# Kernel optimization log

Measured on AMD Instinct MI355X. Metric: run time of the kernel, lower is better.

Reference implementation:

```python
import jax, jax.numpy as jnp
from jax import lax
import numpy as np

C = 64          # in_channel
CL = 32         # latent channels = in_channel // latent_dim
IC = 32         # inter_channel
GH, GW = 8, 8   # grid


def conv1x1(x, W, b):
    # x: [N,C,H,W], W: [O,C], b: [O]
    return jnp.einsum('nchw,oc->nohw', x, W) + b[None, :, None, None]


def maxpool2(x):
    return lax.reduce_window(x, -jnp.inf, lax.max, (1, 1, 2, 2), (1, 1, 2, 2), 'VALID')


def conv3x3(x, W, b):
    y = lax.conv_general_dilated(x, W, (1, 1), ((1, 1), (1, 1)),
                                 dimension_numbers=('NCHW', 'OIHW', 'NCHW'))
    return y + b[None, :, None, None]


def setup_inputs() -> dict:
    key = jax.random.key(0)
    ks = jax.random.split(key, 20)
    s = 0.05
    inp = {
        'x': jax.random.normal(ks[0], (4, C, 256, 256), jnp.float32),
        # Self_Attn_FM params (1x1 convs stored as matrices)
        'Wq': jax.random.normal(ks[1], (CL, C), jnp.float32) * s,
        'bq': jnp.zeros((CL,), jnp.float32),
        'Wk': jax.random.normal(ks[2], (CL, C), jnp.float32) * s,
        'bk': jnp.zeros((CL,), jnp.float32),
        'Wv': jax.random.normal(ks[3], (CL, C), jnp.float32) * s,
        'bv': jnp.zeros((CL,), jnp.float32),
        'Wo': jax.random.normal(ks[4], (C, CL), jnp.float32) * s,
        'bo': jnp.zeros((C,), jnp.float32),
        'gamma': jax.random.normal(ks[5], ()) * 0.5,
        # dense conv blocks: dims 64 -> 96 -> 128, each -> 32
        'W1': jax.random.normal(ks[6], (IC, C, 3, 3), jnp.float32) * s,
        'b1': jnp.zeros((IC,), jnp.float32),
        'W2': jax.random.normal(ks[7], (IC, C + IC, 3, 3), jnp.float32) * s,
        'b2': jnp.zeros((IC,), jnp.float32),
        'W3': jax.random.normal(ks[8], (IC, C + 2 * IC, 3, 3), jnp.float32) * s,
        'b3': jnp.zeros((IC,), jnp.float32),
        # fusion 1x1: (C + 3*IC) -> C
        'Wf': jax.random.normal(ks[9], (C, C + 3 * IC), jnp.float32) * s,
        'bf': jnp.zeros((C,), jnp.float32),
    }
    return inp


def region_non_local(x, Wq, bq, Wk, bk, Wv, bv, Wo, bo, gamma):
    B, Cc, H, W = x.shape
    h, w = H // GH, W // GW
    # split into grid cells, batched: [B*GH*GW, C, h, w]
    cells = x.reshape(B, Cc, GH, h, GW, w).transpose(0, 2, 4, 1, 3, 5)
    cells = cells.reshape(B * GH * GW, Cc, h, w)
    N, L = cells.shape[0], h * w
    q = conv1x1(cells, Wq, bq).reshape(N, CL, L)                 # [N,c,L]
    k = maxpool2(conv1x1(cells, Wk, bk)).reshape(N, CL, L // 4)  # [N,c,L/4]
    v = maxpool2(conv1x1(cells, Wv, bv)).reshape(N, CL, L // 4)
    attn = jax.nn.softmax(jnp.einsum('ncq,nck->nqk', q, k), axis=-1)
    out = jnp.einsum('nck,nqk->ncq', v, attn).reshape(N, CL, h, w)
    out = gamma * conv1x1(out, Wo, bo) + cells
    # regroup cells back to [B,C,H,W]
    out = out.reshape(B, GH, GW, Cc, h, w).transpose(0, 3, 1, 4, 2, 5)
    return out.reshape(B, Cc, H, W)


def reference(x, Wq, bq, Wk, bk, Wv, bv, Wo, bo, gamma,
              W1, b1, W2, b2, W3, b3, Wf, bf):
    f0 = region_non_local(x, Wq, bq, Wk, bk, Wv, bv, Wo, bo, gamma)
    f1 = jax.nn.relu(conv3x3(f0, W1, b1))
    f2 = jax.nn.relu(conv3x3(jnp.concatenate([f0, f1], axis=1), W2, b2))
    f3 = jax.nn.relu(conv3x3(jnp.concatenate([f0, f1, f2], axis=1), W3, b3))
    cat = jnp.concatenate([f0, f1, f2, f3], axis=1)
    out = conv1x1(cat, Wf, bf) + x
    return out
```

## Files before the change

kernel.cpp:

```cpp
#include <hip/hip_runtime.h>


typedef short s16x8 __attribute__((ext_vector_type(8)));
typedef float f32x4 __attribute__((ext_vector_type(4)));
typedef unsigned short ushort_t;

__device__ __forceinline__ unsigned short f2bf(float f) {
  union { float f; unsigned int u; } v; v.f = f;
  unsigned int r = v.u + 0x7fffu + ((v.u >> 16) & 1u);
  return (unsigned short)(r >> 16);
}
__device__ __forceinline__ float bf2f(unsigned short h) {
  union { unsigned int u; float f; } v; v.u = ((unsigned int)h) << 16;
  return v.f;
}

__global__ void repack_kernel(const float* __restrict__ W1, const float* __restrict__ W2,
                              const float* __restrict__ W3, const float* __restrict__ Wf,
                              ushort_t* __restrict__ wc1, ushort_t* __restrict__ wc2,
                              ushort_t* __restrict__ wc3, ushort_t* __restrict__ wff)
{
  const int i = blockIdx.x * 256 + threadIdx.x;
  if (i < 18432) {
    int j = i & 7, o = (i >> 3) & 31, r = i >> 8, tap = r >> 3, kg = r & 7;
    wc1[i] = f2bf(W1[o * 576 + (kg * 8 + j) * 9 + tap]);
  }
  if (i < 27648) {
    int j = i & 7, o = (i >> 3) & 31, r = i >> 8, tap = r / 12, kg = r % 12;
    wc2[i] = f2bf(W2[o * 864 + (kg * 8 + j) * 9 + tap]);
  }
  if (i < 36864) {
    int j = i & 7, o = (i >> 3) & 31, r = i >> 8, tap = r >> 4, kg = r & 15;
    wc3[i] = f2bf(W3[o * 1152 + (kg * 8 + j) * 9 + tap]);
  }
  if (i < 10240) {
    int j = i & 7, o = (i >> 3) & 63, kg = i >> 9;
    wff[i] = f2bf(Wf[o * 160 + kg * 8 + j]);
  }
}

__global__ __launch_bounds__(256, 4) void kvx_kernel(
    const float* __restrict__ x,
    const float* __restrict__ Wk, const float* __restrict__ bk,
    const float* __restrict__ Wv, const float* __restrict__ bv,
    ushort_t* __restrict__ xt, ushort_t* __restrict__ kg, ushort_t* __restrict__ vt)
{
  __shared__ __attribute__((aligned(16))) ushort_t lds[64 * 258];
  __shared__ ushort_t kvs[4][8][64];

  const int bid = blockIdx.x;
  const int n   = bid >> 8;
  const int rem = bid & 255;
  const int pr  = rem >> 1;
  const int xh  = rem & 1;
  const int tid = threadIdx.x, lane = tid & 63, wv = tid >> 6;
  const int quad = lane >> 4, l15 = lane & 15;

  const int y0 = pr * 2;
  const int x0 = xh * 128;
  const int gh = pr >> 4, pyc = pr & 15;

  const float* xblk = x + (size_t)n * (64 * 65536) + (size_t)(y0 * 256 + x0);
  ushort_t*    xtn  = xt + (size_t)n * (65536 * 64);

#pragma unroll 4
  for (int i = 0; i < 16; ++i) {
    const int idx = (i << 8) + tid;
    const int c  = idx >> 6;
    const int r  = (idx >> 5) & 1;
    const int sg = idx & 31;
    const f32x4 v = *(const f32x4*)(xblk + (size_t)c * 65536 + r * 256 + sg * 4);
    const unsigned int lo = (unsigned int)f2bf(v[0]) | ((unsigned int)f2bf(v[1]) << 16);
    const unsigned int hi = (unsigned int)f2bf(v[2]) | ((unsigned int)f2bf(v[3]) << 16);
    const int base = c * 258 + (r << 7) + (sg << 2);
    *(unsigned int*)&lds[base]     = lo;
    *(unsigned int*)&lds[base + 2] = hi;
  }

  s16x8 wkf[2][2], wvf[2][2];
#pragma unroll
  for (int ks = 0; ks < 2; ++ks)
#pragma unroll
    for (int nt = 0; nt < 2; ++nt) {
      const int off = (nt * 16 + l15) * 64 + ks * 32 + quad * 8;
      s16x8 tk, tv;
#pragma unroll
      for (int j = 0; j < 8; ++j) {
        tk[j] = (short)f2bf(Wk[off + j]);
        tv[j] = (short)f2bf(Wv[off + j]);
      }
      wkf[ks][nt] = tk; wvf[ks][nt] = tv;
    }
  float bkv[2], bvv[2];
#pragma unroll
  for (int nt = 0; nt < 2; ++nt) {
    bkv[nt] = bk[nt * 16 + l15];
    bvv[nt] = bv[nt * 16 + l15];
  }

  __syncthreads();

  {
    const int g  = lane & 7;
    const int pa = lane >> 3;
#pragma unroll
    for (int s = 0; s < 8; ++s) {
      const int p = (wv << 6) + (s << 3) + pa;
      s16x8 v;
#pragma unroll
      for (int j = 0; j < 8; ++j) v[j] = (short)lds[(g * 8 + j) * 258 + p];
      const int P = (y0 + (p >> 7)) * 256 + x0 + (p & 127);
      *(s16x8*)(xtn + (size_t)P * 64 + g * 8) = v;
    }
  }

  const f32x4 zf = {0.f, 0.f, 0.f, 0.f};
#pragma unroll
  for (int tt = 0; tt < 2; ++tt) {
    const int t   = wv * 2 + tt;
    const int px0 = t * 16 + l15;

    s16x8 a[2][2];
#pragma unroll
    for (int r = 0; r < 2; ++r)
#pragma unroll
      for (int ks = 0; ks < 2; ++ks) {
        s16x8 v;
#pragma unroll
        for (int j = 0; j < 8; ++j)
          v[j] = (short)lds[(ks * 32 + quad * 8 + j) * 258 + (r << 7) + px0];
        a[r][ks] = v;
      }

    f32x4 kd[2][2], vd[2][2];
#pragma unroll
    for (int r = 0; r < 2; ++r)
#pragma unroll
      for (int nt = 0; nt < 2; ++nt) {
        f32x4 k0 = __builtin_amdgcn_mfma_f32_16x16x32_bf16(a[r][0], wkf[0][nt], zf, 0, 0, 0);
        kd[r][nt] = __builtin_amdgcn_mfma_f32_16x16x32_bf16(a[r][1], wkf[1][nt], k0, 0, 0, 0);
        f32x4 v0 = __builtin_amdgcn_mfma_f32_16x16x32_bf16(a[r][0], wvf[0][nt], zf, 0, 0, 0);
        vd[r][nt] = __builtin_amdgcn_mfma_f32_16x16x32_bf16(a[r][1], wvf[1][nt], v0, 0, 0, 0);
      }

#pragma unroll
    for (int nt = 0; nt < 2; ++nt)
#pragma unroll
      for (int rr = 0; rr < 2; ++rr) {
        const float kp = fmaxf(fmaxf(kd[0][nt][2 * rr], kd[0][nt][2 * rr + 1]),
                               fmaxf(kd[1][nt][2 * rr], kd[1][nt][2 * rr + 1])) + bkv[nt];
        const float vp = fmaxf(fmaxf(vd[0][nt][2 * rr], vd[0][nt][2 * rr + 1]),
                               fmaxf(vd[1][nt][2 * rr], vd[1][nt][2 * rr + 1])) + bvv[nt];
        kvs[wv][quad * 2 + rr][nt * 16 + l15]      = f2bf(kp);
        kvs[wv][quad * 2 + rr][32 + nt * 16 + l15] = f2bf(vp);
      }

    const int gw    = xh * 4 + (t >> 1);
    const int cell  = (n << 6) + (gh << 3) + gw;
    const int kposb = pyc * 16 + (t & 1) * 8;
    if (lane < 32) {
      const s16x8 vv = *(const s16x8*)&kvs[wv][lane >> 2][(lane & 3) * 8];
      *(s16x8*)(kg + ((size_t)(cell << 8) + kposb + (lane >> 2)) * 32 + (lane & 3) * 8) = vv;
    } else {
      const int ch = lane - 32;
      s16x8 vv;
#pragma unroll
      for (int r = 0; r < 8; ++r) vv[r] = (short)kvs[wv][r][32 + ch];
      *(s16x8*)(vt + (size_t)(cell << 13) + ch * 256 + kposb) = vv;
    }
  }
}

__global__ __launch_bounds__(256, 3) void attn_kernel(
    const ushort_t* __restrict__ xt, const ushort_t* __restrict__ kg,
    const ushort_t* __restrict__ vt,
    const float* __restrict__ Wq, const float* __restrict__ bq,
    const float* __restrict__ Wo, const float* __restrict__ bo,
    const float* __restrict__ gamma_p, ushort_t* __restrict__ f0)
{
  __shared__ __attribute__((aligned(16))) ushort_t kl[256 * 36];
  __shared__ __attribute__((aligned(16))) ushort_t vl[32 * 260];
  __shared__ __attribute__((aligned(16))) ushort_t un[4][2176];

  const int bid = blockIdx.x;
  const int cell = bid >> 2;
  const int part = bid & 3;
  const int tid = threadIdx.x, lane = tid & 63, wv = tid >> 6;
  const int quad = lane >> 4, l15 = lane & 15;

  const int n  = cell >> 6;
  const int gh = (cell >> 3) & 7;
  const int gw = cell & 7;
  const int y0 = gh * 32, xc0 = gw * 32;

  const ushort_t* xtn = xt + (size_t)n * (65536 * 64);
  ushort_t*       f0n = f0 + (size_t)n * (65536 * 64);
  const ushort_t* kc  = kg + (size_t)(cell << 8) * 32;
  const ushort_t* vc  = vt + (size_t)(cell << 13);

  for (int idx = tid; idx < 1024; idx += 256) {
    const int kpos = idx >> 2, cg = idx & 3;
    *(s16x8*)&kl[kpos * 36 + cg * 8] = *(const s16x8*)(kc + kpos * 32 + cg * 8);
  }
  for (int idx = tid; idx < 1024; idx += 256) {
    const int ch = idx >> 5, seg = idx & 31;
    *(s16x8*)&vl[ch * 260 + seg * 8] = *(const s16x8*)(vc + ch * 256 + seg * 8);
  }

  const float gamma = gamma_p[0];

  s16x8 wqf[2][2];
#pragma unroll
  for (int ks = 0; ks < 2; ++ks)
#pragma unroll
    for (int nt = 0; nt < 2; ++nt) {
      const float* p = Wq + (nt * 16 + l15) * 64 + ks * 32 + quad * 8;
      s16x8 t;
#pragma unroll
      for (int j = 0; j < 8; ++j) t[j] = (short)f2bf(p[j]);
      wqf[ks][nt] = t;
    }
  s16x8 wof[4];
#pragma unroll
  for (int nt = 0; nt < 4; ++nt) {
    const float* p = Wo + (nt * 16 + l15) * 32 + quad * 8;
    s16x8 t;
#pragma unroll
    for (int j = 0; j < 8; ++j) t[j] = (short)f2bf(p[j]);
    wof[nt] = t;
  }
  float bqv[2]; bqv[0] = bq[l15]; bqv[1] = bq[16 + l15];
  float bov[4];
#pragma unroll
  for (int nt = 0; nt < 4; ++nt) bov[nt] = bo[nt * 16 + l15];

  __syncthreads();

  ushort_t* uw = un[wv];
  const f32x4 zf = {0.f, 0.f, 0.f, 0.f};

#pragma unroll 1
  for (int it = 0; it < 4; ++it) {
    const int mt = part * 16 + wv * 4 + it;
    const int pbase = mt * 16;

    const int p = pbase + l15;
    const int yy = p >> 5, xx = p & 31;
    const size_t pixg = (size_t)((y0 + yy) * 256 + xc0 + xx);

    const s16x8 a0 = *(const s16x8*)(xtn + pixg * 64 + quad * 8);
    const s16x8 a1 = *(const s16x8*)(xtn + pixg * 64 + 32 + quad * 8);
    f32x4 qd0 = zf, qd1 = zf;
    qd0 = __builtin_amdgcn_mfma_f32_16x16x32_bf16(a0, wqf[0][0], qd0, 0, 0, 0);
    qd0 = __builtin_amdgcn_mfma_f32_16x16x32_bf16(a1, wqf[1][0], qd0, 0, 0, 0);
    qd1 = __builtin_amdgcn_mfma_f32_16x16x32_bf16(a0, wqf[0][1], qd1, 0, 0, 0);
    qd1 = __builtin_amdgcn_mfma_f32_16x16x32_bf16(a1, wqf[1][1], qd1, 0, 0, 0);
#pragma unroll
    for (int i = 0; i < 4; ++i) {
      uw[(quad * 4 + i) * 40 + l15]      = f2bf(qd0[i] + bqv[0]);
      uw[(quad * 4 + i) * 40 + 16 + l15] = f2bf(qd1[i] + bqv[1]);
    }
    const s16x8 qa = *(const s16x8*)&uw[l15 * 40 + quad * 8];

    f32x4 S[16];
#pragma unroll
    for (int nt = 0; nt < 16; ++nt) {
      const s16x8 kb = *(const s16x8*)&kl[(nt * 16 + l15) * 36 + quad * 8];
      S[nt] = __builtin_amdgcn_mfma_f32_16x16x32_bf16(qa, kb, zf, 0, 0, 0);
    }

    float rl[4];
#pragma unroll
    for (int i = 0; i < 4; ++i) {
      float m = S[0][i];
#pragma unroll
      for (int nt = 1; nt < 16; ++nt) m = fmaxf(m, S[nt][i]);
#pragma unroll
      for (int d2 = 1; d2 < 16; d2 <<= 1) m = fmaxf(m, __shfl_xor(m, d2, 64));
      float s = 0.f;
#pragma unroll
      for (int nt = 0; nt < 16; ++nt) {
        float e = __expf(S[nt][i] - m);
        S[nt][i] = e;
        s += e;
      }
#pragma unroll
      for (int d2 = 1; d2 < 16; d2 <<= 1) s += __shfl_xor(s, d2, 64);
      rl[i] = s;
    }

    f32x4 O0 = zf, O1 = zf;
#pragma unroll
    for (int hh = 0; hh < 2; ++hh) {
#pragma unroll
      for (int t = 0; t < 8; ++t)
#pragma unroll
        for (int i = 0; i < 4; ++i)
          uw[(quad * 4 + i) * 136 + t * 16 + l15] = f2bf(S[hh * 8 + t][i]);
#pragma unroll
      for (int kk = 0; kk < 4; ++kk) {
        const s16x8 pa = *(const s16x8*)&uw[l15 * 136 + kk * 32 + quad * 8];
        const int kb0 = hh * 128 + kk * 32 + quad * 8;
        const s16x8 vb0 = *(const s16x8*)&vl[l15 * 260 + kb0];
        const s16x8 vb1 = *(const s16x8*)&vl[(16 + l15) * 260 + kb0];
        O0 = __builtin_amdgcn_mfma_f32_16x16x32_bf16(pa, vb0, O0, 0, 0, 0);
        O1 = __builtin_amdgcn_mfma_f32_16x16x32_bf16(pa, vb1, O1, 0, 0, 0);
      }
    }

#pragma unroll
    for (int i = 0; i < 4; ++i) {
      const float inv = 1.0f / rl[i];
      uw[(quad * 4 + i) * 40 + l15]      = f2bf(O0[i] * inv);
      uw[(quad * 4 + i) * 40 + 16 + l15] = f2bf(O1[i] * inv);
    }
    const s16x8 oa = *(const s16x8*)&uw[l15 * 40 + quad * 8];
#pragma unroll
    for (int nt = 0; nt < 4; ++nt) {
      f32x4 D = __builtin_amdgcn_mfma_f32_16x16x32_bf16(oa, wof[nt], zf, 0, 0, 0);
#pragma unroll
      for (int i = 0; i < 4; ++i)
        uw[(quad * 4 + i) * 72 + nt * 16 + l15] = f2bf(gamma * (D[i] + bov[nt]));
    }

    {
      const s16x8 fv0 = *(const s16x8*)&uw[l15 * 72 + quad * 16];
      const s16x8 fv1 = *(const s16x8*)&uw[l15 * 72 + quad * 16 + 8];
      const s16x8 xv0 = *(const s16x8*)(xtn + pixg * 64 + quad * 16);
      const s16x8 xv1 = *(const s16x8*)(xtn + pixg * 64 + quad * 16 + 8);
      s16x8 r0, r1;
#pragma unroll
      for (int j = 0; j < 8; ++j) {
        r0[j] = (short)f2bf(bf2f((unsigned short)fv0[j]) + bf2f((unsigned short)xv0[j]));
        r1[j] = (short)f2bf(bf2f((unsigned short)fv1[j]) + bf2f((unsigned short)xv1[j]));
      }
      *(s16x8*)(f0n + pixg * 64 + quad * 16)     = r0;
      *(s16x8*)(f0n + pixg * 64 + quad * 16 + 8) = r1;
    }
  }
}

template <int NCHUNK>
__global__ __launch_bounds__(256) void conv3_kernel(
    const ushort_t* __restrict__ s0, const ushort_t* __restrict__ s1,
    const ushort_t* __restrict__ s2, const ushort_t* __restrict__ wc,
    const float* __restrict__ bias, ushort_t* __restrict__ outp)
{
  __shared__ __attribute__((aligned(16))) ushort_t tile[612 * 40];

  const int bid = blockIdx.x;
  const int n = bid >> 7;
  const int t = bid & 127;
  const int ty0 = (t >> 3) * 16;
  const int tx0 = (t & 7) * 32;
  const int tid = threadIdx.x, lane = tid & 63, wv = tid >> 6;
  const int quad = lane >> 4, l15 = lane & 15;
  constexpr int Kg = NCHUNK * 4;

  const f32x4 zf = {0.f, 0.f, 0.f, 0.f};
  f32x4 acc[4][2][2];
#pragma unroll
  for (int r = 0; r < 4; ++r)
#pragma unroll
    for (int h = 0; h < 2; ++h) { acc[r][h][0] = zf; acc[r][h][1] = zf; }

  for (int ch = 0; ch < NCHUNK; ++ch) {
    const ushort_t* src; int cstr, cbase;
    if (ch < 2)       { src = s0 + (size_t)n * (65536 * 64); cstr = 64; cbase = ch * 32; }
    else if (ch == 2) { src = s1 + (size_t)n * (65536 * 32); cstr = 32; cbase = 0; }
    else              { src = s2 + (size_t)n * (65536 * 32); cstr = 32; cbase = 0; }

    __syncthreads();
    for (int u = tid; u < 2448; u += 256) {
      const int pix = u >> 2, cg = u & 3;
      const int lr = pix / 34, lc = pix - lr * 34;
      const int gy = ty0 - 1 + lr, gx = tx0 - 1 + lc;
      s16x8 v = {0, 0, 0, 0, 0, 0, 0, 0};
      if ((unsigned)gy < 256u && (unsigned)gx < 256u)
        v = *(const s16x8*)(src + (size_t)(gy * 256 + gx) * cstr + cbase + cg * 8);
      *(s16x8*)&tile[pix * 40 + cg * 8] = v;
    }
    __syncthreads();

#pragma unroll
    for (int tap = 0; tap < 9; ++tap) {
      const int ky = tap / 3, kx = tap - ky * 3;
      const ushort_t* wb = wc + ((size_t)(tap * Kg + ch * 4 + quad) * 32 + l15) * 8;
      const s16x8 b0 = *(const s16x8*)wb;
      const s16x8 b1 = *(const s16x8*)(wb + 128);
#pragma unroll
      for (int r = 0; r < 4; ++r) {
        const int lr = 4 * wv + r + ky;
#pragma unroll
        for (int h = 0; h < 2; ++h) {
          const int lc = h * 16 + l15 + kx;
          const s16x8 a = *(const s16x8*)&tile[(lr * 34 + lc) * 40 + quad * 8];
          acc[r][h][0] = __builtin_amdgcn_mfma_f32_16x16x32_bf16(a, b0, acc[r][h][0], 0, 0, 0);
          acc[r][h][1] = __builtin_amdgcn_mfma_f32_16x16x32_bf16(a, b1, acc[r][h][1], 0, 0, 0);
        }
      }
    }
  }

  const float bv0 = bias[l15], bv1 = bias[16 + l15];
  ushort_t* on = outp + (size_t)n * (65536 * 32);
#pragma unroll
  for (int r = 0; r < 4; ++r) {
    const int gy = ty0 + 4 * wv + r;
#pragma unroll
    for (int h = 0; h < 2; ++h) {
#pragma unroll
      for (int i = 0; i < 4; ++i) {
        const int gx = tx0 + h * 16 + quad * 4 + i;
        ushort_t* op = on + (size_t)(gy * 256 + gx) * 32;
        op[l15]      = f2bf(fmaxf(acc[r][h][0][i] + bv0, 0.f));
        op[16 + l15] = f2bf(fmaxf(acc[r][h][1][i] + bv1, 0.f));
      }
    }
  }
}

__global__ __launch_bounds__(256) void fuse_kernel(
    const ushort_t* __restrict__ f0, const ushort_t* __restrict__ f1,
    const ushort_t* __restrict__ f2, const ushort_t* __restrict__ f3,
    const float* __restrict__ x, const ushort_t* __restrict__ wff,
    const float* __restrict__ bfv, float* __restrict__ out)
{
  __shared__ float tr[4][64 * 17];

  const int tid = threadIdx.x, lane = tid & 63, wv = tid >> 6;
  const int quad = lane >> 4, l15 = lane & 15;

  s16x8 wf[5][4];
#pragma unroll
  for (int ks = 0; ks < 5; ++ks)
#pragma unroll
    for (int nt = 0; nt < 4; ++nt)
      wf[ks][nt] = *(const s16x8*)(wff + ((size_t)((ks * 4 + quad) * 64) + nt * 16 + l15) * 8);
  float bb[4];
#pragma unroll
  for (int nt = 0; nt < 4; ++nt) bb[nt] = bfv[nt * 16 + l15];

  const int wt = blockIdx.x * 4 + wv;
  const f32x4 zf = {0.f, 0.f, 0.f, 0.f};
  float* trw = tr[wv];

  for (int mt = 0; mt < 4; ++mt) {
    const int p0 = wt * 64 + mt * 16;
    const size_t pA = (size_t)(p0 + l15);
    const s16x8 a0 = *(const s16x8*)(f0 + pA * 64 + quad * 8);
    const s16x8 a1 = *(const s16x8*)(f0 + pA * 64 + 32 + quad * 8);
    const s16x8 a2 = *(const s16x8*)(f1 + pA * 32 + quad * 8);
    const s16x8 a3 = *(const s16x8*)(f2 + pA * 32 + quad * 8);
    const s16x8 a4 = *(const s16x8*)(f3 + pA * 32 + quad * 8);

    f32x4 acc[4];
#pragma unroll
    for (int nt = 0; nt < 4; ++nt) {
      f32x4 d = zf;
      d = __builtin_amdgcn_mfma_f32_16x16x32_bf16(a0, wf[0][nt], d, 0, 0, 0);
      d = __builtin_amdgcn_mfma_f32_16x16x32_bf16(a1, wf[1][nt], d, 0, 0, 0);
      d = __builtin_amdgcn_mfma_f32_16x16x32_bf16(a2, wf[2][nt], d, 0, 0, 0);
      d = __builtin_amdgcn_mfma_f32_16x16x32_bf16(a3, wf[3][nt], d, 0, 0, 0);
      d = __builtin_amdgcn_mfma_f32_16x16x32_bf16(a4, wf[4][nt], d, 0, 0, 0);
      acc[nt] = d;
    }

#pragma unroll
    for (int nt = 0; nt < 4; ++nt)
#pragma unroll
      for (int i = 0; i < 4; ++i)
        trw[(nt * 16 + l15) * 17 + quad * 4 + i] = acc[nt][i] + bb[nt];

    const int n = p0 >> 16;
    const int pix0 = p0 & 65535;
    const float* xb = x + (size_t)n * (64 * 65536);
    float* ob = out + (size_t)n * (64 * 65536);
#pragma unroll
    for (int og = 0; og < 16; ++og) {
      const int o = og * 4 + quad;
      const float v = trw[o * 17 + l15];
      const size_t g = (size_t)o * 65536 + pix0 + l15;
      ob[g] = v + xb[g];
    }
  }
}

extern "C" void kernel_launch(void* const* d_in, const int* in_sizes, int n_in,
                              void* d_out, int out_size, void* d_ws, size_t ws_size,
                              hipStream_t stream)
{
  const float* x     = (const float*)d_in[0];
  const float* Wq    = (const float*)d_in[1];
  const float* bq    = (const float*)d_in[2];
  const float* Wk    = (const float*)d_in[3];
  const float* bk    = (const float*)d_in[4];
  const float* Wv    = (const float*)d_in[5];
  const float* bv    = (const float*)d_in[6];
  const float* Wo    = (const float*)d_in[7];
  const float* bo    = (const float*)d_in[8];
  const float* gamma = (const float*)d_in[9];
  const float* W1    = (const float*)d_in[10];
  const float* b1    = (const float*)d_in[11];
  const float* W2    = (const float*)d_in[12];
  const float* b2    = (const float*)d_in[13];
  const float* W3    = (const float*)d_in[14];
  const float* b3    = (const float*)d_in[15];
  const float* Wf    = (const float*)d_in[16];
  const float* bf    = (const float*)d_in[17];

  float* out = (float*)d_out;
  ushort_t* wsu = (ushort_t*)d_ws;

  ushort_t* f0 = wsu;
  ushort_t* f1 = wsu + 16777216;
  ushort_t* f2 = wsu + 25165824;
  ushort_t* f3 = wsu + 33554432;
  ushort_t* xtb = wsu + 16777216;
  ushort_t* kgb = wsu + 33554432;
  ushort_t* vtb = wsu + 35651584;
  ushort_t* wc1 = wsu + 41943040;
  ushort_t* wc2 = wc1 + 18432;
  ushort_t* wc3 = wc2 + 27648;
  ushort_t* wff = wc3 + 36864;

  repack_kernel<<<144, 256, 0, stream>>>(W1, W2, W3, Wf, wc1, wc2, wc3, wff);
  kvx_kernel<<<1024, 256, 0, stream>>>(x, Wk, bk, Wv, bv, xtb, kgb, vtb);
  attn_kernel<<<1024, 256, 0, stream>>>(xtb, kgb, vtb, Wq, bq, Wo, bo, gamma, f0);
  conv3_kernel<2><<<512, 256, 0, stream>>>(f0, f1, f2, wc1, b1, f1);
  conv3_kernel<3><<<512, 256, 0, stream>>>(f0, f1, f2, wc2, b2, f2);
  conv3_kernel<4><<<512, 256, 0, stream>>>(f0, f1, f2, wc3, b3, f3);
  fuse_kernel<<<1024, 256, 0, stream>>>(f0, f1, f2, f3, x, wff, bf, out);
}
```

Baseline: 338.3 us.

## Compute transposed attention scores and feed P to MFMA via shuffles instead of LDS

The attention kernel now computes S^T (keys as rows) so each lane's softmax reduction runs mostly in registers with only two cross-lane shuffles. The probabilities are packed to bf16 with v_cvt_pk_bf16_f32 and routed into the PV MFMA operand layout through lane shuffles rather than an LDS round trip. Blocks grow to 512 threads covering half a cell, which halves the redundant K/V staging into LDS, and Wq/Wo are pre-converted to bf16 in the repack kernel. In exchange there are many more shuffle instructions and register pressure from the packed P array.

```diff
diff --git a/kernel.cpp b/kernel.cpp
--- a/kernel.cpp
+++ b/kernel.cpp
@@ -14,11 +14,18 @@
   union { unsigned int u; float f; } v; v.u = ((unsigned int)h) << 16;
   return v.f;
 }
+__device__ __forceinline__ unsigned int cvtpk(float a, float b) {
+  unsigned int r;
+  asm("v_cvt_pk_bf16_f32 %0, %1, %2" : "=v"(r) : "v"(a), "v"(b));
+  return r;
+}
 
 __global__ void repack_kernel(const float* __restrict__ W1, const float* __restrict__ W2,
                               const float* __restrict__ W3, const float* __restrict__ Wf,
+                              const float* __restrict__ Wq, const float* __restrict__ Wo,
                               ushort_t* __restrict__ wc1, ushort_t* __restrict__ wc2,
-                              ushort_t* __restrict__ wc3, ushort_t* __restrict__ wff)
+                              ushort_t* __restrict__ wc3, ushort_t* __restrict__ wff,
+                              ushort_t* __restrict__ woq, ushort_t* __restrict__ wou)
 {
   const int i = blockIdx.x * 256 + threadIdx.x;
   if (i < 18432) {
@@ -36,6 +43,10 @@
   if (i < 10240) {
     int j = i & 7, o = (i >> 3) & 63, kg = i >> 9;
     wff[i] = f2bf(Wf[o * 160 + kg * 8 + j]);
+  }
+  if (i < 2048) {
+    woq[i] = f2bf(Wq[i]);
+    wou[i] = f2bf(Wo[i]);
   }
 }
 
@@ -171,20 +182,20 @@
   }
 }
 
-__global__ __launch_bounds__(256, 3) void attn_kernel(
+__global__ __launch_bounds__(512, 4) void attn_kernel(
     const ushort_t* __restrict__ xt, const ushort_t* __restrict__ kg,
     const ushort_t* __restrict__ vt,
-    const float* __restrict__ Wq, const float* __restrict__ bq,
-    const float* __restrict__ Wo, const float* __restrict__ bo,
+    const ushort_t* __restrict__ woq, const float* __restrict__ bq,
+    const ushort_t* __restrict__ wou, const float* __restrict__ bo,
     const float* __restrict__ gamma_p, ushort_t* __restrict__ f0)
 {
   __shared__ __attribute__((aligned(16))) ushort_t kl[256 * 36];
-  __shared__ __attribute__((aligned(16))) ushort_t vl[32 * 260];
-  __shared__ __attribute__((aligned(16))) ushort_t un[4][2176];
+  __shared__ __attribute__((aligned(16))) ushort_t vl[32 * 268];
+  __shared__ __attribute__((aligned(16))) ushort_t un[8][1152];
 
   const int bid = blockIdx.x;
-  const int cell = bid >> 2;
-  const int part = bid & 3;
+  const int cell = bid >> 1;
+  const int part = bid & 1;
   const int tid = threadIdx.x, lane = tid & 63, wv = tid >> 6;
   const int quad = lane >> 4, l15 = lane & 15;
 
@@ -198,13 +209,13 @@
   const ushort_t* kc  = kg + (size_t)(cell << 8) * 32;
   const ushort_t* vc  = vt + (size_t)(cell << 13);
 
-  for (int idx = tid; idx < 1024; idx += 256) {
+  for (int idx = tid; idx < 1024; idx += 512) {
     const int kpos = idx >> 2, cg = idx & 3;
     *(s16x8*)&kl[kpos * 36 + cg * 8] = *(const s16x8*)(kc + kpos * 32 + cg * 8);
   }
-  for (int idx = tid; idx < 1024; idx += 256) {
+  for (int idx = tid; idx < 1024; idx += 512) {
     const int ch = idx >> 5, seg = idx & 31;
-    *(s16x8*)&vl[ch * 260 + seg * 8] = *(const s16x8*)(vc + ch * 256 + seg * 8);
+    *(s16x8*)&vl[ch * 268 + seg * 8] = *(const s16x8*)(vc + ch * 256 + seg * 8);
   }
 
   const float gamma = gamma_p[0];
@@ -213,22 +224,8 @@
 #pragma unroll
   for (int ks = 0; ks < 2; ++ks)
 #pragma unroll
-    for (int nt = 0; nt < 2; ++nt) {
-      const float* p = Wq + (nt * 16 + l15) * 64 + ks * 32 + quad * 8;
-      s16x8 t;
-#pragma unroll
-      for (int j = 0; j < 8; ++j) t[j] = (short)f2bf(p[j]);
-      wqf[ks][nt] = t;
-    }
-  s16x8 wof[4];
-#pragma unroll
-  for (int nt = 0; nt < 4; ++nt) {
-    const float* p = Wo + (nt * 16 + l15) * 32 + quad * 8;
-    s16x8 t;
-#pragma unroll
-    for (int j = 0; j < 8; ++j) t[j] = (short)f2bf(p[j]);
-    wof[nt] = t;
-  }
+    for (int nt = 0; nt < 2; ++nt)
+      wqf[ks][nt] = *(const s16x8*)(woq + (nt * 16 + l15) * 64 + ks * 32 + quad * 8);
   float bqv[2]; bqv[0] = bq[l15]; bqv[1] = bq[16 + l15];
   float bov[4];
 #pragma unroll
@@ -239,9 +236,13 @@
   ushort_t* uw = un[wv];
   const f32x4 zf = {0.f, 0.f, 0.f, 0.f};
 
+  const int src0 = ((quad & 1) << 5) + l15;
+  const int src1 = src0 + 16;
+  const int hsel = quad >> 1;
+
 #pragma unroll 1
   for (int it = 0; it < 4; ++it) {
-    const int mt = part * 16 + wv * 4 + it;
+    const int mt = part * 32 + wv * 4 + it;
     const int pbase = mt * 16;
 
     const int p = pbase + l15;
@@ -262,62 +263,73 @@
     }
     const s16x8 qa = *(const s16x8*)&uw[l15 * 40 + quad * 8];
 
-    f32x4 S[16];
+    f32x4 St[16];
 #pragma unroll
     for (int nt = 0; nt < 16; ++nt) {
       const s16x8 kb = *(const s16x8*)&kl[(nt * 16 + l15) * 36 + quad * 8];
-      S[nt] = __builtin_amdgcn_mfma_f32_16x16x32_bf16(qa, kb, zf, 0, 0, 0);
-    }
-
-    float rl[4];
+      St[nt] = __builtin_amdgcn_mfma_f32_16x16x32_bf16(kb, qa, zf, 0, 0, 0);
+    }
+
+    float m = St[0][0];
+#pragma unroll
+    for (int nt = 0; nt < 16; ++nt) {
+      m = fmaxf(m, fmaxf(fmaxf(St[nt][0], St[nt][1]), fmaxf(St[nt][2], St[nt][3])));
+    }
+    m = fmaxf(m, __shfl_xor(m, 16, 64));
+    m = fmaxf(m, __shfl_xor(m, 32, 64));
+    float s = 0.f;
+    unsigned int pku[32];
+#pragma unroll
+    for (int nt = 0; nt < 16; ++nt) {
+      const float e0 = __expf(St[nt][0] - m);
+      const float e1 = __expf(St[nt][1] - m);
+      const float e2 = __expf(St[nt][2] - m);
+      const float e3 = __expf(St[nt][3] - m);
+      s += (e0 + e1) + (e2 + e3);
+      pku[2 * nt]     = cvtpk(e0, e1);
+      pku[2 * nt + 1] = cvtpk(e2, e3);
+    }
+    s += __shfl_xor(s, 16, 64);
+    s += __shfl_xor(s, 32, 64);
+
+    f32x4 O0 = zf, O1 = zf;
+#pragma unroll
+    for (int kk = 0; kk < 8; ++kk) {
+      const int A0 = __shfl((int)pku[4 * kk + 0], src0, 64);
+      const int B0 = __shfl((int)pku[4 * kk + 2], src0, 64);
+      const int A1 = __shfl((int)pku[4 * kk + 1], src0, 64);
+      const int B1 = __shfl((int)pku[4 * kk + 3], src0, 64);
+      const int A2 = __shfl((int)pku[4 * kk + 0], src1, 64);
+      const int B2 = __shfl((int)pku[4 * kk + 2], src1, 64);
+      const int A3 = __shfl((int)pku[4 * kk + 1], src1, 64);
+      const int B3 = __shfl((int)pku[4 * kk + 3], src1, 64);
+      union { int w[4]; s16x8 v; } pa;
+      pa.w[0] = hsel ? B0 : A0;
+      pa.w[1] = hsel ? B1 : A1;
+      pa.w[2] = hsel ? B2 : A2;
+      pa.w[3] = hsel ? B3 : A3;
+      const int kb0 = kk * 32 + quad * 8;
+      const s16x8 vb0 = *(const s16x8*)&vl[l15 * 268 + kb0];
+      const s16x8 vb1 = *(const s16x8*)&vl[(16 + l15) * 268 + kb0];
+      O0 = __builtin_amdgcn_mfma_f32_16x16x32_bf16(pa.v, vb0, O0, 0, 0, 0);
+      O1 = __builtin_amdgcn_mfma_f32_16x16x32_bf16(pa.v, vb1, O1, 0, 0, 0);
+    }
+
+    float rv[4];
+#pragma unroll
+    for (int i = 0; i < 4; ++i) rv[i] = __shfl(s, quad * 4 + i, 64);
+
 #pragma unroll
     for (int i = 0; i < 4; ++i) {
-      float m = S[0][i];
-#pragma unroll
-      for (int nt = 1; nt < 16; ++nt) m = fmaxf(m, S[nt][i]);
-#pragma unroll
-      for (int d2 = 1; d2 < 16; d2 <<= 1) m = fmaxf(m, __shfl_xor(m, d2, 64));
-      float s = 0.f;
-#pragma unroll
-      for (int nt = 0; nt < 16; ++nt) {
-        float e = __expf(S[nt][i] - m);
-        S[nt][i] = e;
-        s += e;
-      }
-#pragma unroll
-      for (int d2 = 1; d2 < 16; d2 <<= 1) s += __shfl_xor(s, d2, 64);
-      rl[i] = s;
-    }
-
-    f32x4 O0 = zf, O1 = zf;
-#pragma unroll
-    for (int hh = 0; hh < 2; ++hh) {
-#pragma unroll
-      for (int t = 0; t < 8; ++t)
-#pragma unroll
-        for (int i = 0; i < 4; ++i)
-          uw[(quad * 4 + i) * 136 + t * 16 + l15] = f2bf(S[hh * 8 + t][i]);
-#pragma unroll
-      for (int kk = 0; kk < 4; ++kk) {
-        const s16x8 pa = *(const s16x8*)&uw[l15 * 136 + kk * 32 + quad * 8];
-        const int kb0 = hh * 128 + kk * 32 + quad * 8;
-        const s16x8 vb0 = *(const s16x8*)&vl[l15 * 260 + kb0];
-        const s16x8 vb1 = *(const s16x8*)&vl[(16 + l15) * 260 + kb0];
-        O0 = __builtin_amdgcn_mfma_f32_16x16x32_bf16(pa, vb0, O0, 0, 0, 0);
-        O1 = __builtin_amdgcn_mfma_f32_16x16x32_bf16(pa, vb1, O1, 0, 0, 0);
-      }
-    }
-
-#pragma unroll
-    for (int i = 0; i < 4; ++i) {
-      const float inv = 1.0f / rl[i];
+      const float inv = 1.0f / rv[i];
       uw[(quad * 4 + i) * 40 + l15]      = f2bf(O0[i] * inv);
       uw[(quad * 4 + i) * 40 + 16 + l15] = f2bf(O1[i] * inv);
     }
     const s16x8 oa = *(const s16x8*)&uw[l15 * 40 + quad * 8];
 #pragma unroll
     for (int nt = 0; nt < 4; ++nt) {
-      f32x4 D = __builtin_amdgcn_mfma_f32_16x16x32_bf16(oa, wof[nt], zf, 0, 0, 0);
+      const s16x8 wofn = *(const s16x8*)(wou + (nt * 16 + l15) * 32 + quad * 8);
+      f32x4 D = __builtin_amdgcn_mfma_f32_16x16x32_bf16(oa, wofn, zf, 0, 0, 0);
 #pragma unroll
       for (int i = 0; i < 4; ++i)
         uw[(quad * 4 + i) * 72 + nt * 16 + l15] = f2bf(gamma * (D[i] + bov[nt]));
@@ -328,14 +340,18 @@
       const s16x8 fv1 = *(const s16x8*)&uw[l15 * 72 + quad * 16 + 8];
       const s16x8 xv0 = *(const s16x8*)(xtn + pixg * 64 + quad * 16);
       const s16x8 xv1 = *(const s16x8*)(xtn + pixg * 64 + quad * 16 + 8);
-      s16x8 r0, r1;
-#pragma unroll
-      for (int j = 0; j < 8; ++j) {
-        r0[j] = (short)f2bf(bf2f((unsigned short)fv0[j]) + bf2f((unsigned short)xv0[j]));
-        r1[j] = (short)f2bf(bf2f((unsigned short)fv1[j]) + bf2f((unsigned short)xv1[j]));
-      }
-      *(s16x8*)(f0n + pixg * 64 + quad * 16)     = r0;
-      *(s16x8*)(f0n + pixg * 64 + quad * 16 + 8) = r1;
+      union { unsigned int w[4]; s16x8 v; } r0, r1;
+#pragma unroll
+      for (int k = 0; k < 4; ++k) {
+        const float p0 = bf2f((unsigned short)fv0[2 * k])     + bf2f((unsigned short)xv0[2 * k]);
+        const float p1 = bf2f((unsigned short)fv0[2 * k + 1]) + bf2f((unsigned short)xv0[2 * k + 1]);
+        const float p2 = bf2f((unsigned short)fv1[2 * k])     + bf2f((unsigned short)xv1[2 * k]);
+        const float p3 = bf2f((unsigned short)fv1[2 * k + 1]) + bf2f((unsigned short)xv1[2 * k + 1]);
+        r0.w[k] = cvtpk(p0, p1);
+        r1.w[k] = cvtpk(p2, p3);
+      }
+      *(s16x8*)(f0n + pixg * 64 + quad * 16)     = r0.v;
+      *(s16x8*)(f0n + pixg * 64 + quad * 16 + 8) = r1.v;
     }
   }
 }
@@ -523,10 +539,13 @@
   ushort_t* wc2 = wc1 + 18432;
   ushort_t* wc3 = wc2 + 27648;
   ushort_t* wff = wc3 + 36864;
-
-  repack_kernel<<<144, 256, 0, stream>>>(W1, W2, W3, Wf, wc1, wc2, wc3, wff);
+  ushort_t* woq = wff + 10240;
+  ushort_t* wou = woq + 2048;
+
+  repack_kernel<<<144, 256, 0, stream>>>(W1, W2, W3, Wf, Wq, Wo,
+                                         wc1, wc2, wc3, wff, woq, wou);
   kvx_kernel<<<1024, 256, 0, stream>>>(x, Wk, bk, Wv, bv, xtb, kgb, vtb);
-  attn_kernel<<<1024, 256, 0, stream>>>(xtb, kgb, vtb, Wq, bq, Wo, bo, gamma, f0);
+  attn_kernel<<<512, 512, 0, stream>>>(xtb, kgb, vtb, woq, bq, wou, bo, gamma, f0);
   conv3_kernel<2><<<512, 256, 0, stream>>>(f0, f1, f2, wc1, b1, f1);
   conv3_kernel<3><<<512, 256, 0, stream>>>(f0, f1, f2, wc2, b2, f2);
   conv3_kernel<4><<<512, 256, 0, stream>>>(f0, f1, f2, wc3, b3, f3);
```

Result: slower. 363.4 us (+7.4%).
